# Performance work log

Hardware: AMD Instinct MI355X
Metric: run time of the kernel (lower is better)

The kernel has to match this reference:

```python
import jax, jax.numpy as jnp
import numpy as np

N = 20000          # nodes
E = 320000         # edges
C = 64             # channel multiplicity (64x0e node feats)
NATTR = 10         # node attr (species one-hot) dim
EDGE_FEAT = 8      # radial bessel features
L_DIMS = (1, 3, 5) # irrep dims for l = 0,1,2
RAD = [64, 64, 64]
AVG_NEIGH = 16.0
NUM_L = len(L_DIMS)


def setup_inputs() -> dict:
    key = jax.random.key(0)
    ks = jax.random.split(key, 12)
    node_attrs = jax.random.uniform(ks[0], (N, NATTR), dtype=jnp.float32)
    node_feats = jax.random.normal(ks[1], (N, C), dtype=jnp.float32)
    edge_attrs = jax.random.normal(ks[2], (E, sum(L_DIMS)), dtype=jnp.float32)
    edge_feats = jax.random.normal(ks[3], (E, EDGE_FEAT), dtype=jnp.float32)
    edge_index = jax.random.randint(ks[4], (2, E), 0, N, dtype=jnp.int64)
    # linear1: o3.Linear(64x0e -> 64x0e)
    W_lin1 = jax.random.normal(ks[5], (C, C), dtype=jnp.float32)
    # radial MLP: FullyConnectedNet([8,64,64,64,192], Identity)
    W_r0 = jax.random.normal(ks[6], (EDGE_FEAT, RAD[0]), dtype=jnp.float32)
    W_r1 = jax.random.normal(ks[7], (RAD[0], RAD[1]), dtype=jnp.float32)
    W_r2 = jax.random.normal(ks[8], (RAD[1], RAD[2]), dtype=jnp.float32)
    W_r3 = jax.random.normal(ks[9], (RAD[2], NUM_L * C), dtype=jnp.float32)
    # post-aggregation linear: o3.Linear(64x0e+64x1o+64x2e -> same), per-l 64x64 mix
    W_msg = jax.random.normal(ks[10], (NUM_L, C, C), dtype=jnp.float32)
    # skip_tp: FullyConnectedTensorProduct(64x0e, 10x0e -> 64x0e), 'uvw'
    W_skip = jax.random.normal(ks[11], (C, NATTR, C), dtype=jnp.float32)
    return {
        "node_attrs": node_attrs, "node_feats": node_feats,
        "edge_attrs": edge_attrs, "edge_feats": edge_feats,
        "edge_index": edge_index,
        "W_lin1": W_lin1, "W_r0": W_r0, "W_r1": W_r1, "W_r2": W_r2,
        "W_r3": W_r3, "W_msg": W_msg, "W_skip": W_skip,
    }


def reference(node_attrs, node_feats, edge_attrs, edge_feats, edge_index,
              W_lin1, W_r0, W_r1, W_r2, W_r3, W_msg, W_skip):
    sender, receiver = edge_index[0], edge_index[1]
    num_nodes = node_feats.shape[0]
    num_edges = edge_feats.shape[0]

    # linear1 (o3.Linear on scalars): fan_in normalized
    h = node_feats @ (W_lin1 / np.float32(np.sqrt(C)))           # [N, C]

    # radial MLP (e3nn FullyConnectedNet, identity activation)
    w = edge_feats
    for W in (W_r0, W_r1, W_r2, W_r3):
        w = w @ (W / np.float32(np.sqrt(W.shape[0])))
    tp_w = w.reshape(num_edges, NUM_L, C)                        # per-l 'uvu' weights

    # edge gather + weighted tensor product (0e x l -> l per channel)
    xs = h[sender]                                               # [E, C]
    blocks = []
    off = 0
    for l, d in enumerate(L_DIMS):
        y_l = edge_attrs[:, off:off + d]                         # [E, d]
        m_l = (xs * tp_w[:, l, :])[:, :, None] * y_l[:, None, :] # [E, C, d]
        blocks.append(m_l.reshape(num_edges, C * d))
        off += d
    mji = jnp.concatenate(blocks, axis=-1)                       # [E, C*9]

    # scatter-sum to receivers
    msg = jax.ops.segment_sum(mji, receiver, num_segments=num_nodes)  # [N, C*9]

    # per-l linear mix + avg-neighbor norm, then reshape_irreps -> [N, C, 9]
    out_blocks = []
    off = 0
    for l, d in enumerate(L_DIMS):
        m_l = msg[:, off:off + C * d].reshape(num_nodes, C, d)
        o_l = jnp.einsum('num,uv->nvm', m_l, W_msg[l]) / np.float32(np.sqrt(C))
        out_blocks.append(o_l)
        off += C * d
    out = jnp.concatenate(out_blocks, axis=-1) / np.float32(AVG_NEIGH)  # [N, C, 9]

    # self connection: FullyConnectedTensorProduct(64x0e, 10x0e -> 64x0e)
    sc = jnp.einsum('nu,nv,uvw->nw', h, node_attrs, W_skip) / np.float32(np.sqrt(C * NATTR))
    return out, sc
```

## Files before the change

### kernel.cpp

```cpp
#include <hip/hip_runtime.h>

#define N_NODES 20000
#define N_EDGES 320000
#define C 64
#define NATTR 10
#define MSG_DIM 576
#define WC_COLS 192
#define PRE 12

__global__ void node_linear(const float* __restrict__ nf,
                            const float* __restrict__ W,
                            float* __restrict__ h,
                            int* __restrict__ counts) {
    const int t = threadIdx.x;
    if (blockIdx.x < 79) {
        const int i = blockIdx.x * 256 + t;
        if (i < N_NODES) counts[i] = 0;
    }
    __shared__ float Ws[64 * 64];
    __shared__ float row[4][64];
    const int lane = t & 63, wv = t >> 6;
    for (int i = t; i < 4096; i += 256) Ws[i] = W[i] * 0.125f;
    __syncthreads();
    const int base = blockIdx.x * 16;
    for (int it = 0; it < 4; ++it) {
        int n = base + it * 4 + wv;
        if (n >= N_NODES) break;
        row[wv][lane] = nf[(size_t)n * 64 + lane];
        float acc = 0.f;
        #pragma unroll
        for (int k = 0; k < 64; ++k) acc += row[wv][k] * Ws[k * 64 + lane];
        h[(size_t)n * 64 + lane] = acc;
    }
}

__global__ void hist_kernel(const int* __restrict__ eidx, int* __restrict__ counts) {
    const int e = blockIdx.x * 256 + threadIdx.x;
    if (e < N_EDGES) atomicAdd(&counts[eidx[N_EDGES + e]], 1);
}

#define SCAN_PER 20
__global__ __launch_bounds__(1024) void scan_radial_kernel(
        const int* __restrict__ counts,
        int* __restrict__ start, int* __restrict__ cursor,
        const float* __restrict__ Wr0, const float* __restrict__ Wr1,
        const float* __restrict__ Wr2, const float* __restrict__ Wr3,
        float* __restrict__ Wc, int* __restrict__ snd_pad) {
    __shared__ int wsum[16];
    __shared__ float T[8 * 64];
    __shared__ float T2[8 * 64];
    const int t = threadIdx.x, lane = t & 63, w = t >> 6;
    const float s0r = 0.35355339059327373f;
    const float s1r = 0.125f;

    const int base = t * SCAN_PER;
    int v[SCAN_PER];
    int s = 0;
    #pragma unroll
    for (int j = 0; j < SCAN_PER; ++j) {
        const int idx = base + j;
        v[j] = (idx < N_NODES) ? counts[idx] : 0;
        s += v[j];
    }
    int sc = s;
    #pragma unroll
    for (int off = 1; off < 64; off <<= 1) {
        int up = __shfl_up(sc, off);
        if (lane >= off) sc += up;
    }
    if (lane == 63) wsum[w] = sc;
    if (t < 16) snd_pad[t] = 0;
    for (int i = t; i < 8 * 64; i += 1024) {
        int r = i >> 6, c = i & 63;
        float acc = 0.f;
        for (int k = 0; k < 64; ++k) acc += Wr0[r * 64 + k] * Wr1[k * 64 + c];
        T[i] = acc * (s0r * s1r);
    }
    __syncthreads();
    if (t == 0) {
        int a = 0;
        #pragma unroll
        for (int i = 0; i < 16; ++i) { int x = wsum[i]; wsum[i] = a; a += x; }
    }
    for (int i = t; i < 8 * 64; i += 1024) {
        int r = i >> 6, c = i & 63;
        float acc = 0.f;
        for (int k = 0; k < 64; ++k) acc += T[r * 64 + k] * Wr2[k * 64 + c];
        T2[i] = acc * s1r;
    }
    __syncthreads();
    int a = wsum[w] + (sc - s);
    #pragma unroll
    for (int j = 0; j < SCAN_PER; ++j) {
        const int idx = base + j;
        if (idx < N_NODES) {
            start[idx] = a;
            cursor[idx] = a;
            a += v[j];
        }
    }
    for (int i = t; i < 8 * WC_COLS; i += 1024) {
        int r = i / WC_COLS, c = i % WC_COLS;
        float acc = 0.f;
        for (int k = 0; k < 64; ++k) acc += T2[r * 64 + k] * Wr3[k * WC_COLS + c];
        Wc[i] = acc * s1r;
    }
}

__global__ void scatter_build(const int* __restrict__ eidx,
                              const float* __restrict__ ef,
                              const float* __restrict__ ea,
                              int* __restrict__ cursor,
                              int* __restrict__ snd_s,
                              float* __restrict__ ef_s,
                              float* __restrict__ ea_s) {
    const int e = blockIdx.x * 256 + threadIdx.x;
    if (e >= N_EDGES) return;
    const int r = eidx[N_EDGES + e];
    const int pos = atomicAdd(&cursor[r], 1);
    snd_s[pos] = eidx[e];
    const float4* s4 = reinterpret_cast<const float4*>(ef + (size_t)e * 8);
    float4* d4 = reinterpret_cast<float4*>(ef_s + (size_t)pos * 8);
    d4[0] = s4[0];
    d4[1] = s4[1];
    const float* y = ea + (size_t)e * 9;
    float4* o4 = reinterpret_cast<float4*>(ea_s + (size_t)pos * 12);
    o4[0] = make_float4(y[0], y[1], y[2], y[3]);
    o4[1] = make_float4(y[4], y[5], y[6], y[7]);
    o4[2] = make_float4(y[8], 0.f, 0.f, 0.f);
}

__global__ __launch_bounds__(256) void gather_sorted(
                              const float* __restrict__ ef_s,
                              const float* __restrict__ ea_s,
                              const int* __restrict__ snd_s,
                              const float* __restrict__ h,
                              const float* __restrict__ Wc,
                              const int* __restrict__ start,
                              const int* __restrict__ counts,
                              float* __restrict__ msg) {
    __shared__ float part[2][9][64];
    const int t = threadIdx.x, lane = t & 63, wv = t >> 6;
    const int g = wv >> 1;
    const int half = wv & 1;
    const int n = blockIdx.x * 2 + g;

    float wc0[8], wc1[8], wc2[8];
    #pragma unroll
    for (int k = 0; k < 8; ++k) {
        wc0[k] = Wc[k * WC_COLS + lane];
        wc1[k] = Wc[k * WC_COLS + 64 + lane];
        wc2[k] = Wc[k * WC_COLS + 128 + lane];
    }

    float p0 = 0.f;
    float p1[3] = {0.f, 0.f, 0.f};
    float p2[5] = {0.f, 0.f, 0.f, 0.f, 0.f};

    if (n < N_NODES) {
        const int s0 = start[n], cnt = counts[n];
        const int jbeg = half ? (cnt >> 1) : 0;
        const int jend = half ? cnt : (cnt >> 1);
        const int m = jend - jbeg;
        const int base = s0 + jbeg;

        if (m > 0) {
            const int P = (m < PRE) ? m : PRE;
            int snd[PRE];
            #pragma unroll
            for (int b = 0; b < PRE; ++b) snd[b] = snd_s[base + b];
            float xs[PRE];
            #pragma unroll
            for (int b = 0; b < PRE; ++b) {
                const int sb = (b < P) ? snd[b] : snd[0];
                xs[b] = h[(size_t)sb * 64 + lane];
            }
            #pragma unroll
            for (int jj = 0; jj < PRE / 2; ++jj) {
                const int j = jj * 2;
                if (j < P) {
                    const bool has2 = (j + 1 < P);
                    const int j1 = has2 ? (j + 1) : j;
                    const float gate1 = has2 ? 1.f : 0.f;
                    const float4* q0e = reinterpret_cast<const float4*>(ef_s + (size_t)(base + j) * 8);
                    const float4* q1e = reinterpret_cast<const float4*>(ef_s + (size_t)(base + j1) * 8);
                    const float4* q0a = reinterpret_cast<const float4*>(ea_s + (size_t)(base + j) * 12);
                    const float4* q1a = reinterpret_cast<const float4*>(ea_s + (size_t)(base + j1) * 12);
                    const float4 e00 = q0e[0], e01 = q0e[1];
                    const float4 e10 = q1e[0], e11 = q1e[1];
                    const float4 a00 = q0a[0], a01 = q0a[1], a02 = q0a[2];
                    const float4 a10 = q1a[0], a11 = q1a[1], a12 = q1a[2];
                    const float xa = xs[j];
                    const float xb = (has2 ? xs[j + 1] : 0.f) * gate1;
                    {
                        const float* fk = reinterpret_cast<const float*>(&e00);
                        const float* gk = reinterpret_cast<const float*>(&e01);
                        float w0 = fk[0] * wc0[0], w1 = fk[0] * wc1[0], w2 = fk[0] * wc2[0];
                        #pragma unroll
                        for (int k = 1; k < 4; ++k) {
                            w0 += fk[k] * wc0[k]; w1 += fk[k] * wc1[k]; w2 += fk[k] * wc2[k];
                        }
                        #pragma unroll
                        for (int k = 0; k < 4; ++k) {
                            w0 += gk[k] * wc0[k + 4]; w1 += gk[k] * wc1[k + 4]; w2 += gk[k] * wc2[k + 4];
                        }
                        const float b0 = xa * w0, b1 = xa * w1, b2 = xa * w2;
                        p0    += b0 * a00.x;
                        p1[0] += b1 * a00.y; p1[1] += b1 * a00.z; p1[2] += b1 * a00.w;
                        p2[0] += b2 * a01.x; p2[1] += b2 * a01.y; p2[2] += b2 * a01.z;
                        p2[3] += b2 * a01.w; p2[4] += b2 * a02.x;
                    }
                    {
                        const float* fk = reinterpret_cast<const float*>(&e10);
                        const float* gk = reinterpret_cast<const float*>(&e11);
                        float w0 = fk[0] * wc0[0], w1 = fk[0] * wc1[0], w2 = fk[0] * wc2[0];
                        #pragma unroll
                        for (int k = 1; k < 4; ++k) {
                            w0 += fk[k] * wc0[k]; w1 += fk[k] * wc1[k]; w2 += fk[k] * wc2[k];
                        }
                        #pragma unroll
                        for (int k = 0; k < 4; ++k) {
                            w0 += gk[k] * wc0[k + 4]; w1 += gk[k] * wc1[k + 4]; w2 += gk[k] * wc2[k + 4];
                        }
                        const float b0 = xb * w0, b1 = xb * w1, b2 = xb * w2;
                        p0    += b0 * a10.x;
                        p1[0] += b1 * a10.y; p1[1] += b1 * a10.z; p1[2] += b1 * a10.w;
                        p2[0] += b2 * a11.x; p2[1] += b2 * a11.y; p2[2] += b2 * a11.z;
                        p2[3] += b2 * a11.w; p2[4] += b2 * a12.x;
                    }
                }
            }
            for (int j = PRE; j < m; ++j) {
                const size_t r0 = (size_t)(base + j);
                const int snd_t = snd_s[r0];
                const float4* pf = reinterpret_cast<const float4*>(ef_s + r0 * 8);
                const float4 fa = pf[0], fb = pf[1];
                const float4* py = reinterpret_cast<const float4*>(ea_s + r0 * 12);
                const float4 ya = py[0], yb = py[1], yc = py[2];
                const float xs_t = h[(size_t)snd_t * 64 + lane];
                const float* fk = reinterpret_cast<const float*>(&fa);
                const float* gk = reinterpret_cast<const float*>(&fb);
                float w0 = fk[0] * wc0[0], w1 = fk[0] * wc1[0], w2 = fk[0] * wc2[0];
                #pragma unroll
                for (int k = 1; k < 4; ++k) {
                    w0 += fk[k] * wc0[k]; w1 += fk[k] * wc1[k]; w2 += fk[k] * wc2[k];
                }
                #pragma unroll
                for (int k = 0; k < 4; ++k) {
                    w0 += gk[k] * wc0[k + 4]; w1 += gk[k] * wc1[k + 4]; w2 += gk[k] * wc2[k + 4];
                }
                const float b0 = xs_t * w0, b1 = xs_t * w1, b2 = xs_t * w2;
                p0    += b0 * ya.x;
                p1[0] += b1 * ya.y; p1[1] += b1 * ya.z; p1[2] += b1 * ya.w;
                p2[0] += b2 * yb.x; p2[1] += b2 * yb.y; p2[2] += b2 * yb.z;
                p2[3] += b2 * yb.w; p2[4] += b2 * yc.x;
            }
        }
    }

    if (half) {
        part[g][0][lane] = p0;
        #pragma unroll
        for (int m2 = 0; m2 < 3; ++m2) part[g][1 + m2][lane] = p1[m2];
        #pragma unroll
        for (int m2 = 0; m2 < 5; ++m2) part[g][4 + m2][lane] = p2[m2];
    }
    __syncthreads();
    if (!half && n < N_NODES) {
        float* mrow = msg + (size_t)n * MSG_DIM;
        mrow[lane] = p0 + part[g][0][lane];
        #pragma unroll
        for (int m2 = 0; m2 < 3; ++m2)
            mrow[64 + lane * 3 + m2] = p1[m2] + part[g][1 + m2][lane];
        #pragma unroll
        for (int m2 = 0; m2 < 5; ++m2)
            mrow[256 + lane * 5 + m2] = p2[m2] + part[g][4 + m2][lane];
    }
}

__global__ __launch_bounds__(256) void out_transform(
        const float* __restrict__ Wmsg,
        float* __restrict__ out) {
    __shared__ float WL[3 * 64 * 64];
    __shared__ __align__(16) float stage[8 * MSG_DIM];
    const int t = threadIdx.x, lane = t & 63, wv = t >> 6;
    for (int i = t; i < 3 * 64 * 64; i += 256) WL[i] = Wmsg[i];

    {
        const float4* src = reinterpret_cast<const float4*>(
            out + (size_t)blockIdx.x * 8 * MSG_DIM);
        float4* dst = reinterpret_cast<float4*>(stage);
        #pragma unroll
        for (int i = 0; i < 4; ++i) dst[t + 256 * i] = src[t + 256 * i];
        if (t < 128) dst[t + 1024] = src[t + 1024];
    }
    __syncthreads();
    const float scale = 1.f / 128.f;

    const int r0 = wv * 2;
    const float* rowA = stage + (size_t)r0 * MSG_DIM;
    const float* rowB = rowA + MSG_DIM;
    float oA[9] = {0.f, 0.f, 0.f, 0.f, 0.f, 0.f, 0.f, 0.f, 0.f};
    float oB[9] = {0.f, 0.f, 0.f, 0.f, 0.f, 0.f, 0.f, 0.f, 0.f};

    #pragma unroll 1
    for (int u8 = 0; u8 < 8; ++u8) {
        const int u0 = u8 * 8;
        float w0[8], w1[8], w2[8];
        #pragma unroll
        for (int j = 0; j < 8; ++j) {
            w0[j] = WL[(u0 + j) * 64 + lane];
            w1[j] = WL[4096 + (u0 + j) * 64 + lane];
            w2[j] = WL[8192 + (u0 + j) * 64 + lane];
        }
        #pragma unroll
        for (int rr = 0; rr < 2; ++rr) {
            const float* row = rr ? rowB : rowA;
            float* o = rr ? oB : oA;
            float c0[8], c1[24], c2[40];
            {
                const float4* p = reinterpret_cast<const float4*>(row + u0);
                #pragma unroll
                for (int q = 0; q < 2; ++q) {
                    float4 v = p[q];
                    c0[q * 4 + 0] = v.x; c0[q * 4 + 1] = v.y;
                    c0[q * 4 + 2] = v.z; c0[q * 4 + 3] = v.w;
                }
            }
            {
                const float4* p = reinterpret_cast<const float4*>(row + 64 + u0 * 3);
                #pragma unroll
                for (int q = 0; q < 6; ++q) {
                    float4 v = p[q];
                    c1[q * 4 + 0] = v.x; c1[q * 4 + 1] = v.y;
                    c1[q * 4 + 2] = v.z; c1[q * 4 + 3] = v.w;
                }
            }
            {
                const float4* p = reinterpret_cast<const float4*>(row + 256 + u0 * 5);
                #pragma unroll
                for (int q = 0; q < 10; ++q) {
                    float4 v = p[q];
                    c2[q * 4 + 0] = v.x; c2[q * 4 + 1] = v.y;
                    c2[q * 4 + 2] = v.z; c2[q * 4 + 3] = v.w;
                }
            }
            #pragma unroll
            for (int j = 0; j < 8; ++j) {
                o[0] += c0[j] * w0[j];
                #pragma unroll
                for (int m = 0; m < 3; ++m) o[1 + m] += c1[j * 3 + m] * w1[j];
                #pragma unroll
                for (int m = 0; m < 5; ++m) o[4 + m] += c2[j * 5 + m] * w2[j];
            }
        }
    }
    float* opA = out + ((size_t)blockIdx.x * 8 + r0) * MSG_DIM + lane * 9;
    float* opB = opA + MSG_DIM;
    #pragma unroll
    for (int m = 0; m < 9; ++m) opA[m] = oA[m] * scale;
    #pragma unroll
    for (int m = 0; m < 9; ++m) opB[m] = oB[m] * scale;
}

__global__ __launch_bounds__(256) void skip_kernel(
                            const float* __restrict__ h,
                            const float* __restrict__ attrs,
                            const float* __restrict__ Wskip,
                            float* __restrict__ sc) {
    __shared__ float hl[32 * 64];
    const int t = threadIdx.x, lane = t & 63, wv = t >> 6;
    const int nb = blockIdx.x * 32;
    for (int i = t; i < 32 * 64; i += 256) hl[i] = h[(size_t)(nb + (i >> 6)) * 64 + (i & 63)];
    __syncthreads();

    float alr[8][NATTR];
    #pragma unroll
    for (int i = 0; i < 8; ++i) {
        const float* ap = attrs + (size_t)(nb + wv + 4 * i) * NATTR;
        #pragma unroll
        for (int v = 0; v < NATTR; ++v) alr[i][v] = ap[v];
    }

    float acc[8] = {0.f, 0.f, 0.f, 0.f, 0.f, 0.f, 0.f, 0.f};
    #pragma unroll 1
    for (int u4 = 0; u4 < 16; ++u4) {
        const int u0 = u4 * 4;
        float4 hu[8];
        #pragma unroll
        for (int i = 0; i < 8; ++i)
            hu[i] = *reinterpret_cast<const float4*>(&hl[(wv + 4 * i) * 64 + u0]);
        #pragma unroll
        for (int uu = 0; uu < 4; ++uu) {
            float tmp[8] = {0.f, 0.f, 0.f, 0.f, 0.f, 0.f, 0.f, 0.f};
            #pragma unroll
            for (int v = 0; v < NATTR; ++v) {
                const float wk = Wskip[((u0 + uu) * NATTR + v) * 64 + lane];
                #pragma unroll
                for (int i = 0; i < 8; ++i) tmp[i] += alr[i][v] * wk;
            }
            #pragma unroll
            for (int i = 0; i < 8; ++i) {
                const float huv = (uu == 0) ? hu[i].x : (uu == 1) ? hu[i].y
                                 : (uu == 2) ? hu[i].z : hu[i].w;
                acc[i] += huv * tmp[i];
            }
        }
    }
    const float scale = 0.03952847075210474f;
    #pragma unroll
    for (int i = 0; i < 8; ++i)
        sc[(size_t)(nb + wv + 4 * i) * 64 + lane] = acc[i] * scale;
}

extern "C" void kernel_launch(void* const* d_in, const int* in_sizes, int n_in,
                              void* d_out, int out_size, void* d_ws, size_t ws_size,
                              hipStream_t stream) {
    const float* node_attrs = (const float*)d_in[0];
    const float* node_feats = (const float*)d_in[1];
    const float* edge_attrs = (const float*)d_in[2];
    const float* edge_feats = (const float*)d_in[3];
    const int*   edge_index = (const int*)d_in[4];
    const float* W_lin1 = (const float*)d_in[5];
    const float* W_r0 = (const float*)d_in[6];
    const float* W_r1 = (const float*)d_in[7];
    const float* W_r2 = (const float*)d_in[8];
    const float* W_r3 = (const float*)d_in[9];
    const float* W_msg = (const float*)d_in[10];
    const float* W_skip = (const float*)d_in[11];

    float* out = (float*)d_out;
    float* sc  = out + (size_t)N_NODES * MSG_DIM;

    float* wsf = (float*)d_ws;
    float* Wc = wsf;
    float* h  = wsf + 2048;
    int* wsi   = (int*)(wsf + 2048 + (size_t)N_NODES * 64);
    int* counts = wsi;
    int* start  = wsi + N_NODES;
    int* cursor = wsi + 2 * N_NODES;
    int*   snd_s = wsi + 3 * N_NODES;
    float* ef_s  = (float*)(snd_s + N_EDGES + 16);
    float* ea_s  = ef_s + (size_t)N_EDGES * 8;

    node_linear<<<1250, 256, 0, stream>>>(node_feats, W_lin1, h, counts);
    hist_kernel<<<(N_EDGES + 255) / 256, 256, 0, stream>>>(edge_index, counts);
    scan_radial_kernel<<<1, 1024, 0, stream>>>(counts, start, cursor,
                                               W_r0, W_r1, W_r2, W_r3, Wc,
                                               snd_s + N_EDGES);
    scatter_build<<<(N_EDGES + 255) / 256, 256, 0, stream>>>(
        edge_index, edge_feats, edge_attrs, cursor, snd_s, ef_s, ea_s);

    gather_sorted<<<(N_NODES + 1) / 2, 256, 0, stream>>>(
        ef_s, ea_s, snd_s, h, Wc, start, counts, out);

    out_transform<<<2500, 256, 0, stream>>>(W_msg, out);
    skip_kernel<<<625, 256, 0, stream>>>(h, node_attrs, W_skip, sc);
}
```

Before: 252.8 us.

## Fuse per-l output mixing into the sorted gather kernel

The gather kernel now combines the two half-wave partial sums in shared memory and applies the per-l 64x64 W_msg mix directly, writing the final [N,C,9] output. The separate out_transform kernel is removed, along with the round trip of the 576-wide msg buffer through global memory. Each wave pair splits the mix: one handles l=0,1 and the other l=2, reading W_msg from global or L2 per lane instead of from staged shared memory. The node bounds check is dropped because the grid exactly covers N_NODES/2.

Result: faster. 241.2 us (-4.6%).

```diff
diff --git a/kernel.cpp b/kernel.cpp
--- a/kernel.cpp
+++ b/kernel.cpp
@@ -130,15 +130,16 @@
     o4[2] = make_float4(y[8], 0.f, 0.f, 0.f);
 }
 
-__global__ __launch_bounds__(256) void gather_sorted(
+__global__ __launch_bounds__(256) void gather_fused(
                               const float* __restrict__ ef_s,
                               const float* __restrict__ ea_s,
                               const int* __restrict__ snd_s,
                               const float* __restrict__ h,
                               const float* __restrict__ Wc,
+                              const float* __restrict__ Wmsg,
                               const int* __restrict__ start,
                               const int* __restrict__ counts,
-                              float* __restrict__ msg) {
+                              float* __restrict__ out) {
     __shared__ float part[2][9][64];
     const int t = threadIdx.x, lane = t & 63, wv = t >> 6;
     const int g = wv >> 1;
@@ -157,7 +158,7 @@
     float p1[3] = {0.f, 0.f, 0.f};
     float p2[5] = {0.f, 0.f, 0.f, 0.f, 0.f};
 
-    if (n < N_NODES) {
+    {
         const int s0 = start[n], cnt = counts[n];
         const int jbeg = half ? (cnt >> 1) : 0;
         const int jend = half ? cnt : (cnt >> 1);
@@ -266,101 +267,49 @@
         for (int m2 = 0; m2 < 5; ++m2) part[g][4 + m2][lane] = p2[m2];
     }
     __syncthreads();
-    if (!half && n < N_NODES) {
-        float* mrow = msg + (size_t)n * MSG_DIM;
-        mrow[lane] = p0 + part[g][0][lane];
-        #pragma unroll
-        for (int m2 = 0; m2 < 3; ++m2)
-            mrow[64 + lane * 3 + m2] = p1[m2] + part[g][1 + m2][lane];
-        #pragma unroll
-        for (int m2 = 0; m2 < 5; ++m2)
-            mrow[256 + lane * 5 + m2] = p2[m2] + part[g][4 + m2][lane];
-    }
-}
-
-__global__ __launch_bounds__(256) void out_transform(
-        const float* __restrict__ Wmsg,
-        float* __restrict__ out) {
-    __shared__ float WL[3 * 64 * 64];
-    __shared__ __align__(16) float stage[8 * MSG_DIM];
-    const int t = threadIdx.x, lane = t & 63, wv = t >> 6;
-    for (int i = t; i < 3 * 64 * 64; i += 256) WL[i] = Wmsg[i];
-
-    {
-        const float4* src = reinterpret_cast<const float4*>(
-            out + (size_t)blockIdx.x * 8 * MSG_DIM);
-        float4* dst = reinterpret_cast<float4*>(stage);
-        #pragma unroll
-        for (int i = 0; i < 4; ++i) dst[t + 256 * i] = src[t + 256 * i];
-        if (t < 128) dst[t + 1024] = src[t + 1024];
-    }
-    __syncthreads();
+    if (!half) {
+        part[g][0][lane] += p0;
+        #pragma unroll
+        for (int m2 = 0; m2 < 3; ++m2) part[g][1 + m2][lane] += p1[m2];
+        #pragma unroll
+        for (int m2 = 0; m2 < 5; ++m2) part[g][4 + m2][lane] += p2[m2];
+    }
+    __syncthreads();
+
     const float scale = 1.f / 128.f;
-
-    const int r0 = wv * 2;
-    const float* rowA = stage + (size_t)r0 * MSG_DIM;
-    const float* rowB = rowA + MSG_DIM;
-    float oA[9] = {0.f, 0.f, 0.f, 0.f, 0.f, 0.f, 0.f, 0.f, 0.f};
-    float oB[9] = {0.f, 0.f, 0.f, 0.f, 0.f, 0.f, 0.f, 0.f, 0.f};
-
-    #pragma unroll 1
-    for (int u8 = 0; u8 < 8; ++u8) {
-        const int u0 = u8 * 8;
-        float w0[8], w1[8], w2[8];
-        #pragma unroll
-        for (int j = 0; j < 8; ++j) {
-            w0[j] = WL[(u0 + j) * 64 + lane];
-            w1[j] = WL[4096 + (u0 + j) * 64 + lane];
-            w2[j] = WL[8192 + (u0 + j) * 64 + lane];
+    float* op = out + (size_t)n * MSG_DIM + lane * 9;
+    if (!half) {
+        float o0 = 0.f, o1 = 0.f, o2 = 0.f, o3 = 0.f;
+        #pragma unroll 8
+        for (int u = 0; u < 64; ++u) {
+            const float wv0 = Wmsg[u * 64 + lane];
+            const float wv1 = Wmsg[4096 + u * 64 + lane];
+            o0 += part[g][0][u] * wv0;
+            o1 += part[g][1][u] * wv1;
+            o2 += part[g][2][u] * wv1;
+            o3 += part[g][3][u] * wv1;
         }
-        #pragma unroll
-        for (int rr = 0; rr < 2; ++rr) {
-            const float* row = rr ? rowB : rowA;
-            float* o = rr ? oB : oA;
-            float c0[8], c1[24], c2[40];
-            {
-                const float4* p = reinterpret_cast<const float4*>(row + u0);
-                #pragma unroll
-                for (int q = 0; q < 2; ++q) {
-                    float4 v = p[q];
-                    c0[q * 4 + 0] = v.x; c0[q * 4 + 1] = v.y;
-                    c0[q * 4 + 2] = v.z; c0[q * 4 + 3] = v.w;
-                }
-            }
-            {
-                const float4* p = reinterpret_cast<const float4*>(row + 64 + u0 * 3);
-                #pragma unroll
-                for (int q = 0; q < 6; ++q) {
-                    float4 v = p[q];
-                    c1[q * 4 + 0] = v.x; c1[q * 4 + 1] = v.y;
-                    c1[q * 4 + 2] = v.z; c1[q * 4 + 3] = v.w;
-                }
-            }
-            {
-                const float4* p = reinterpret_cast<const float4*>(row + 256 + u0 * 5);
-                #pragma unroll
-                for (int q = 0; q < 10; ++q) {
-                    float4 v = p[q];
-                    c2[q * 4 + 0] = v.x; c2[q * 4 + 1] = v.y;
-                    c2[q * 4 + 2] = v.z; c2[q * 4 + 3] = v.w;
-                }
-            }
-            #pragma unroll
-            for (int j = 0; j < 8; ++j) {
-                o[0] += c0[j] * w0[j];
-                #pragma unroll
-                for (int m = 0; m < 3; ++m) o[1 + m] += c1[j * 3 + m] * w1[j];
-                #pragma unroll
-                for (int m = 0; m < 5; ++m) o[4 + m] += c2[j * 5 + m] * w2[j];
-            }
+        op[0] = o0 * scale;
+        op[1] = o1 * scale;
+        op[2] = o2 * scale;
+        op[3] = o3 * scale;
+    } else {
+        float o4 = 0.f, o5 = 0.f, o6 = 0.f, o7 = 0.f, o8 = 0.f;
+        #pragma unroll 8
+        for (int u = 0; u < 64; ++u) {
+            const float wv2 = Wmsg[8192 + u * 64 + lane];
+            o4 += part[g][4][u] * wv2;
+            o5 += part[g][5][u] * wv2;
+            o6 += part[g][6][u] * wv2;
+            o7 += part[g][7][u] * wv2;
+            o8 += part[g][8][u] * wv2;
         }
-    }
-    float* opA = out + ((size_t)blockIdx.x * 8 + r0) * MSG_DIM + lane * 9;
-    float* opB = opA + MSG_DIM;
-    #pragma unroll
-    for (int m = 0; m < 9; ++m) opA[m] = oA[m] * scale;
-    #pragma unroll
-    for (int m = 0; m < 9; ++m) opB[m] = oB[m] * scale;
+        op[4] = o4 * scale;
+        op[5] = o5 * scale;
+        op[6] = o6 * scale;
+        op[7] = o7 * scale;
+        op[8] = o8 * scale;
+    }
 }
 
 __global__ __launch_bounds__(256) void skip_kernel(
@@ -451,9 +400,8 @@
     scatter_build<<<(N_EDGES + 255) / 256, 256, 0, stream>>>(
         edge_index, edge_feats, edge_attrs, cursor, snd_s, ef_s, ea_s);
 
-    gather_sorted<<<(N_NODES + 1) / 2, 256, 0, stream>>>(
-        ef_s, ea_s, snd_s, h, Wc, start, counts, out);
-
-    out_transform<<<2500, 256, 0, stream>>>(W_msg, out);
+    gather_fused<<<N_NODES / 2, 256, 0, stream>>>(
+        ef_s, ea_s, snd_s, h, Wc, W_msg, start, counts, out);
+
     skip_kernel<<<625, 256, 0, stream>>>(h, node_attrs, W_skip, sc);
 }
```

## Fuse edge histogram into node linear kernel and read Wmsg directly in out_transform

Applied to the files above, without the earlier changes.

Merges the histogram atomics into the node-linear kernel (1250 blocks x 256 threads covers exactly E edges) and moves zeroing of counts to a hipMemsetAsync, which removes one kernel launch. The out_transform kernel stops staging the 48KB W_msg in shared memory and instead reads weights from global/L2 in chunks of 4, using direct float4 loads from the staged rows. This cuts LDS use, which may raise occupancy, and drops the weight-copy prologue, at the cost of more global weight reads per block.

Measured after the change: 248.7 us. About the same (-1.6%).

```diff
diff --git a/kernel.cpp b/kernel.cpp
--- a/kernel.cpp
+++ b/kernel.cpp
@@ -8,14 +8,15 @@
 #define WC_COLS 192
 #define PRE 12
 
-__global__ void node_linear(const float* __restrict__ nf,
-                            const float* __restrict__ W,
-                            float* __restrict__ h,
-                            int* __restrict__ counts) {
+__global__ void node_linear_hist(const float* __restrict__ nf,
+                                 const float* __restrict__ W,
+                                 float* __restrict__ h,
+                                 const int* __restrict__ eidx,
+                                 int* __restrict__ counts) {
     const int t = threadIdx.x;
-    if (blockIdx.x < 79) {
-        const int i = blockIdx.x * 256 + t;
-        if (i < N_NODES) counts[i] = 0;
+    {
+        const int e = blockIdx.x * 256 + t;
+        atomicAdd(&counts[eidx[N_EDGES + e]], 1);
     }
     __shared__ float Ws[64 * 64];
     __shared__ float row[4][64];
@@ -32,11 +33,6 @@
         for (int k = 0; k < 64; ++k) acc += row[wv][k] * Ws[k * 64 + lane];
         h[(size_t)n * 64 + lane] = acc;
     }
-}
-
-__global__ void hist_kernel(const int* __restrict__ eidx, int* __restrict__ counts) {
-    const int e = blockIdx.x * 256 + threadIdx.x;
-    if (e < N_EDGES) atomicAdd(&counts[eidx[N_EDGES + e]], 1);
 }
 
 #define SCAN_PER 20
@@ -71,9 +67,9 @@
     if (lane == 63) wsum[w] = sc;
     if (t < 16) snd_pad[t] = 0;
     for (int i = t; i < 8 * 64; i += 1024) {
-        int r = i >> 6, c = i & 63;
+        int r = i >> 6, c2 = i & 63;
         float acc = 0.f;
-        for (int k = 0; k < 64; ++k) acc += Wr0[r * 64 + k] * Wr1[k * 64 + c];
+        for (int k = 0; k < 64; ++k) acc += Wr0[r * 64 + k] * Wr1[k * 64 + c2];
         T[i] = acc * (s0r * s1r);
     }
     __syncthreads();
@@ -83,9 +79,9 @@
         for (int i = 0; i < 16; ++i) { int x = wsum[i]; wsum[i] = a; a += x; }
     }
     for (int i = t; i < 8 * 64; i += 1024) {
-        int r = i >> 6, c = i & 63;
+        int r = i >> 6, c2 = i & 63;
         float acc = 0.f;
-        for (int k = 0; k < 64; ++k) acc += T[r * 64 + k] * Wr2[k * 64 + c];
+        for (int k = 0; k < 64; ++k) acc += T[r * 64 + k] * Wr2[k * 64 + c2];
         T2[i] = acc * s1r;
     }
     __syncthreads();
@@ -100,9 +96,9 @@
         }
     }
     for (int i = t; i < 8 * WC_COLS; i += 1024) {
-        int r = i / WC_COLS, c = i % WC_COLS;
+        int r = i / WC_COLS, c2 = i % WC_COLS;
         float acc = 0.f;
-        for (int k = 0; k < 64; ++k) acc += T2[r * 64 + k] * Wr3[k * WC_COLS + c];
+        for (int k = 0; k < 64; ++k) acc += T2[r * 64 + k] * Wr3[k * WC_COLS + c2];
         Wc[i] = acc * s1r;
     }
 }
@@ -281,11 +277,8 @@
 __global__ __launch_bounds__(256) void out_transform(
         const float* __restrict__ Wmsg,
         float* __restrict__ out) {
-    __shared__ float WL[3 * 64 * 64];
     __shared__ __align__(16) float stage[8 * MSG_DIM];
     const int t = threadIdx.x, lane = t & 63, wv = t >> 6;
-    for (int i = t; i < 3 * 64 * 64; i += 256) WL[i] = Wmsg[i];
-
     {
         const float4* src = reinterpret_cast<const float4*>(
             out + (size_t)blockIdx.x * 8 * MSG_DIM);
@@ -304,55 +297,37 @@
     float oB[9] = {0.f, 0.f, 0.f, 0.f, 0.f, 0.f, 0.f, 0.f, 0.f};
 
     #pragma unroll 1
-    for (int u8 = 0; u8 < 8; ++u8) {
-        const int u0 = u8 * 8;
-        float w0[8], w1[8], w2[8];
-        #pragma unroll
-        for (int j = 0; j < 8; ++j) {
-            w0[j] = WL[(u0 + j) * 64 + lane];
-            w1[j] = WL[4096 + (u0 + j) * 64 + lane];
-            w2[j] = WL[8192 + (u0 + j) * 64 + lane];
+    for (int c = 0; c < 16; ++c) {
+        const int u0 = c * 4;
+        float w0[4], w1[4], w2[4];
+        #pragma unroll
+        for (int k = 0; k < 4; ++k) {
+            w0[k] = Wmsg[(u0 + k) * 64 + lane];
+            w1[k] = Wmsg[4096 + (u0 + k) * 64 + lane];
+            w2[k] = Wmsg[8192 + (u0 + k) * 64 + lane];
         }
         #pragma unroll
         for (int rr = 0; rr < 2; ++rr) {
             const float* row = rr ? rowB : rowA;
             float* o = rr ? oB : oA;
-            float c0[8], c1[24], c2[40];
-            {
-                const float4* p = reinterpret_cast<const float4*>(row + u0);
-                #pragma unroll
-                for (int q = 0; q < 2; ++q) {
-                    float4 v = p[q];
-                    c0[q * 4 + 0] = v.x; c0[q * 4 + 1] = v.y;
-                    c0[q * 4 + 2] = v.z; c0[q * 4 + 3] = v.w;
-                }
-            }
-            {
-                const float4* p = reinterpret_cast<const float4*>(row + 64 + u0 * 3);
-                #pragma unroll
-                for (int q = 0; q < 6; ++q) {
-                    float4 v = p[q];
-                    c1[q * 4 + 0] = v.x; c1[q * 4 + 1] = v.y;
-                    c1[q * 4 + 2] = v.z; c1[q * 4 + 3] = v.w;
-                }
-            }
-            {
-                const float4* p = reinterpret_cast<const float4*>(row + 256 + u0 * 5);
-                #pragma unroll
-                for (int q = 0; q < 10; ++q) {
-                    float4 v = p[q];
-                    c2[q * 4 + 0] = v.x; c2[q * 4 + 1] = v.y;
-                    c2[q * 4 + 2] = v.z; c2[q * 4 + 3] = v.w;
-                }
-            }
-            #pragma unroll
-            for (int j = 0; j < 8; ++j) {
-                o[0] += c0[j] * w0[j];
-                #pragma unroll
-                for (int m = 0; m < 3; ++m) o[1 + m] += c1[j * 3 + m] * w1[j];
-                #pragma unroll
-                for (int m = 0; m < 5; ++m) o[4 + m] += c2[j * 5 + m] * w2[j];
-            }
+            const float4 c0 = *reinterpret_cast<const float4*>(row + u0);
+            const float4 c1a = *reinterpret_cast<const float4*>(row + 64 + u0 * 3);
+            const float4 c1b = *reinterpret_cast<const float4*>(row + 64 + u0 * 3 + 4);
+            const float4 c1c = *reinterpret_cast<const float4*>(row + 64 + u0 * 3 + 8);
+            const float4 c2a = *reinterpret_cast<const float4*>(row + 256 + u0 * 5);
+            const float4 c2b = *reinterpret_cast<const float4*>(row + 256 + u0 * 5 + 4);
+            const float4 c2c = *reinterpret_cast<const float4*>(row + 256 + u0 * 5 + 8);
+            const float4 c2d = *reinterpret_cast<const float4*>(row + 256 + u0 * 5 + 12);
+            const float4 c2e = *reinterpret_cast<const float4*>(row + 256 + u0 * 5 + 16);
+            o[0] += c0.x * w0[0] + c0.y * w0[1] + c0.z * w0[2] + c0.w * w0[3];
+            o[1] += c1a.x * w1[0] + c1a.w * w1[1] + c1b.z * w1[2] + c1c.y * w1[3];
+            o[2] += c1a.y * w1[0] + c1b.x * w1[1] + c1b.w * w1[2] + c1c.z * w1[3];
+            o[3] += c1a.z * w1[0] + c1b.y * w1[1] + c1c.x * w1[2] + c1c.w * w1[3];
+            o[4] += c2a.x * w2[0] + c2b.y * w2[1] + c2c.z * w2[2] + c2d.w * w2[3];
+            o[5] += c2a.y * w2[0] + c2b.z * w2[1] + c2c.w * w2[2] + c2e.x * w2[3];
+            o[6] += c2a.z * w2[0] + c2b.w * w2[1] + c2d.x * w2[2] + c2e.y * w2[3];
+            o[7] += c2a.w * w2[0] + c2c.x * w2[1] + c2d.y * w2[2] + c2e.z * w2[3];
+            o[8] += c2b.x * w2[0] + c2c.y * w2[1] + c2d.z * w2[2] + c2e.w * w2[3];
         }
     }
     float* opA = out + ((size_t)blockIdx.x * 8 + r0) * MSG_DIM + lane * 9;
@@ -443,8 +418,9 @@
     float* ef_s  = (float*)(snd_s + N_EDGES + 16);
     float* ea_s  = ef_s + (size_t)N_EDGES * 8;
 
-    node_linear<<<1250, 256, 0, stream>>>(node_feats, W_lin1, h, counts);
-    hist_kernel<<<(N_EDGES + 255) / 256, 256, 0, stream>>>(edge_index, counts);
+    hipMemsetAsync(counts, 0, N_NODES * sizeof(int), stream);
+    node_linear_hist<<<1250, 256, 0, stream>>>(node_feats, W_lin1, h,
+                                               edge_index, counts);
     scan_radial_kernel<<<1, 1024, 0, stream>>>(counts, start, cursor,
                                                W_r0, W_r1, W_r2, W_r3, Wc,
                                                snd_s + N_EDGES);
```
